# Performance work log

Hardware: AMD Instinct MI355X
Metric: run time of the kernel (lower is better)

## Reference

```python
import jax, jax.numpy as jnp
import numpy as np

B, S, D = 4, 4096, 1024          # batch, seq, d_model
K, H, A = 32, 4, 2               # mem_key_dim, mem_hashes, mem_assoc
T, NB = 65536, 16                # mem_buckets = 2**NB
Dm, Tv = 64, 32                  # mem_dim, mem_vsa_dim
READ_TEMP, VSA_W = 1.0, 1.0
TANH_SCALE, BETA, NOV_THR = 1.0, 1.0, 0.0
WRITE_THR, ETA = 0.5, 0.1


def setup_inputs() -> dict:
    key = jax.random.key(0)
    k = jax.random.split(key, 12)
    s = 0.02
    return {
        "u": jax.random.normal(k[0], (B, S, D), jnp.float32),
        "Wq": jax.random.normal(k[1], (K, D), jnp.float32) * s,
        "Ww": jax.random.normal(k[2], (K, D), jnp.float32) * s,
        "Wv": jax.random.normal(k[3], (Dm, D), jnp.float32) * s,
        "Wout": jax.random.normal(k[4], (D, Dm), jnp.float32) * s,
        "Wg": jax.random.normal(k[5], (1, D), jnp.float32) * s,
        "bg": jnp.zeros((1,), jnp.float32),
        "R": jax.random.normal(k[6], (H, K, NB), jnp.float32),
        "P": jax.random.normal(k[7], (Tv, K), jnp.float32) / np.float32(np.sqrt(K)),
        "mem_keys": jax.random.normal(k[8], (T, A, K), jnp.float32),
        "mem_vals": jax.random.normal(k[9], (T, A, Dm), jnp.float32),
        "mem_tags": jnp.tanh(jax.random.normal(k[10], (T, A, Tv), jnp.float32)),
    }


def reference(u, Wq, Ww, Wv, Wout, Wg, bg, R, P, mem_keys, mem_vals, mem_tags):
    # --- routing (BitRouter): sign bits of random projections -> bucket per hash ---
    q = jnp.einsum('bsd,kd->bsk', u, Wq)                              # query tag
    bits = (jnp.einsum('bsk,hkn->bshn', q, R) > 0).astype(jnp.int32)
    pw = 2 ** jnp.arange(NB, dtype=jnp.int32)
    idx = jnp.sum(bits * pw, axis=-1)                                 # [B,S,H] in [0,T)

    # --- read: gather bucket slots, key + VSA-tag scores, softmax over H*A ---
    Kg, Vg, Tg = mem_keys[idx], mem_vals[idx], mem_tags[idx]          # [B,S,H,A,*]
    score = jnp.einsum('bsk,bshak->bsha', q, Kg) / jnp.sqrt(jnp.float32(K))
    qt = jnp.tanh(TANH_SCALE * jnp.einsum('bsk,tk->bst', q, P))       # VSA tag of query
    score = score + VSA_W * jnp.einsum('bst,bshat->bsha', qt, Tg) / Tv
    attn = jax.nn.softmax((score / READ_TEMP).reshape(B, S, H * A), axis=-1)
    attn = attn.reshape(B, S, H, A)
    read = jnp.einsum('bsha,bshad->bsd', attn, Vg)                    # [B,S,Dm]
    y = jnp.einsum('bsm,dm->bsd', read, Wout)                         # [B,S,D]

    # --- write: gate + VSA novelty, blend best-matching slot, scatter-add ---
    wk = jnp.einsum('bsd,kd->bsk', u, Ww)
    v = jnp.einsum('bsd,md->bsm', u, Wv)
    g = jax.nn.sigmoid(jnp.einsum('bsd,od->bso', u, Wg) + bg)[..., 0]  # [B,S]
    wt = jnp.tanh(TANH_SCALE * jnp.einsum('bsk,tk->bst', wk, P))
    match = jnp.einsum('bst,bshat->bsha', wt, Tg) / Tv
    slot = jnp.argmax(match, axis=-1)                                  # [B,S,H]
    nov = jax.nn.sigmoid(BETA * (NOV_THR - jnp.max(match, axis=-1)))   # novelty gate
    w = ETA * (g * (g > WRITE_THR))[..., None] * nov                   # [B,S,H]
    flat = (idx * A + slot).reshape(-1)                                # [B*S*H]

    def blend(table, gathered, target, dim):
        cur = jnp.take_along_axis(gathered, slot[..., None, None], axis=3)[..., 0, :]
        d = (w[..., None] * (target[:, :, None, :] - cur)).reshape(-1, dim)
        return table.reshape(T * A, dim).at[flat].add(d).reshape(T, A, dim)

    new_keys = blend(mem_keys, Kg, wk, K)
    new_vals = blend(mem_vals, Vg, v, Dm)
    new_tags = blend(mem_tags, Tg, wt, Tv)
    return y, new_keys, new_vals, new_tags
```

## Files before the change

### kernel.cpp

```cpp
#include <hip/hip_runtime.h>
#include <hip/hip_bf16.h>
#include <cstdint>

#define BB 4
#define SS 4096
#define DD 1024
#define KK 32
#define HH 4
#define AA 2
#define TT 65536
#define NBB 16
#define DM 64
#define TV 32
#define MTOK (BB*SS)

__global__ __launch_bounds__(512) void proj_kernel(
    const float* __restrict__ u, const float* __restrict__ Wq,
    const float* __restrict__ Ww, const float* __restrict__ Wv,
    const float* __restrict__ Wg,
    float* __restrict__ q_o, float* __restrict__ wk_o,
    float* __restrict__ v_o, float* __restrict__ g_o)
{
    __shared__ float u_t[64][68];
    __shared__ float w_t[129][68];
    const int t  = threadIdx.x;
    const int m0 = blockIdx.x * 64;
    const int ty = t >> 5;
    const int tx = t & 31;

    float acc[4][5];
#pragma unroll
    for (int i = 0; i < 4; i++)
#pragma unroll
        for (int j = 0; j < 5; j++) acc[i][j] = 0.f;

    for (int k0 = 0; k0 < DD; k0 += 64) {
        __syncthreads();
#pragma unroll
        for (int i = 0; i < 2; i++) {
            int e = t + i * 512;
            int r = e >> 4, cv = e & 15;
            float4 val = *(const float4*)(u + (size_t)(m0 + r) * DD + k0 + cv * 4);
            *(float4*)&u_t[r][cv * 4] = val;
        }
#pragma unroll
        for (int i = 0; i < 5; i++) {
            int e = t + i * 512;
            if (e < 2064) {
                int c = e >> 4, cv = e & 15;
                const float* wrow = (c < 32)  ? (Wq + (size_t)c * DD)
                                  : (c < 64)  ? (Ww + (size_t)(c - 32) * DD)
                                  : (c < 128) ? (Wv + (size_t)(c - 64) * DD)
                                              : Wg;
                float4 val = *(const float4*)(wrow + k0 + cv * 4);
                *(float4*)&w_t[c][cv * 4] = val;
            }
        }
        __syncthreads();
#pragma unroll
        for (int k4 = 0; k4 < 16; k4++) {
            float4 a4[4], b4[5];
#pragma unroll
            for (int i = 0; i < 4; i++) a4[i] = *(const float4*)&u_t[ty * 4 + i][k4 * 4];
#pragma unroll
            for (int j = 0; j < 4; j++) b4[j] = *(const float4*)&w_t[tx + j * 32][k4 * 4];
            b4[4] = *(const float4*)&w_t[128][k4 * 4];
#pragma unroll
            for (int i = 0; i < 4; i++)
#pragma unroll
                for (int j = 0; j < 5; j++) {
                    acc[i][j] = fmaf(a4[i].x, b4[j].x, acc[i][j]);
                    acc[i][j] = fmaf(a4[i].y, b4[j].y, acc[i][j]);
                    acc[i][j] = fmaf(a4[i].z, b4[j].z, acc[i][j]);
                    acc[i][j] = fmaf(a4[i].w, b4[j].w, acc[i][j]);
                }
        }
    }
#pragma unroll
    for (int i = 0; i < 4; i++) {
        int m = m0 + ty * 4 + i;
#pragma unroll
        for (int j = 0; j < 5; j++) {
            int c = tx + j * 32;
            if (c < 32)        q_o[(size_t)m * KK + c]        = acc[i][j];
            else if (c < 64)   wk_o[(size_t)m * KK + (c - 32)] = acc[i][j];
            else if (c < 128)  v_o[(size_t)m * DM + (c - 64)]  = acc[i][j];
            else if (tx == 0)  g_o[m] = acc[i][4];
        }
    }
}

__global__ __launch_bounds__(256) void route_kernel(
    const float* __restrict__ R, const float* __restrict__ P,
    const float* __restrict__ mem_keys, const float* __restrict__ mem_vals,
    const float* __restrict__ mem_tags, const float* __restrict__ bg,
    const float* __restrict__ q_i, const float* __restrict__ wk_i,
    const float* __restrict__ g_i,
    float* __restrict__ read_o, float* __restrict__ wt_o,
    int* __restrict__ idx_o, int* __restrict__ slot_o, float* __restrict__ w_o)
{
    __shared__ float R_s[HH * KK * NBB];
    __shared__ float P_s[TV][KK + 1];
    __shared__ float q_s[4][KK], wk_s[4][KK], qt_s[4][TV], wt_s[4][TV];
    __shared__ float kg_s[4][8][KK], tg_s[4][8][TV], vg_s[4][8][DM];
    __shared__ float sc_s[4][8], mt_s[4][8];
    __shared__ int   idx_s[4][HH];

    const int t    = threadIdx.x;
    const int wid  = t >> 6;
    const int lane = t & 63;
    const int tok  = blockIdx.x * 4 + wid;

    for (int e = t; e < HH * KK * NBB; e += 256) R_s[e] = R[e];
    for (int e = t; e < TV * KK; e += 256) P_s[e >> 5][e & 31] = P[e];

    if (lane < 32) q_s[wid][lane] = q_i[(size_t)tok * KK + lane];
    else           wk_s[wid][lane - 32] = wk_i[(size_t)tok * KK + (lane - 32)];
    __syncthreads();

    {
        int h = lane >> 4, n = lane & 15;
        float s = 0.f;
#pragma unroll
        for (int k = 0; k < KK; k++) s = fmaf(q_s[wid][k], R_s[h * (KK * NBB) + k * NBB + n], s);
        unsigned long long m = __ballot(s > 0.f);
        if (n == 0) {
            int idx = (int)((m >> (h * 16)) & 0xFFFFull);
            idx_s[wid][h] = idx;
            idx_o[(size_t)tok * HH + h] = idx;
        }
    }
    if (lane < 32) {
        float s = 0.f;
#pragma unroll
        for (int k = 0; k < KK; k++) s = fmaf(q_s[wid][k], P_s[lane][k], s);
        qt_s[wid][lane] = tanhf(s);
    } else {
        int t2 = lane - 32;
        float s = 0.f;
#pragma unroll
        for (int k = 0; k < KK; k++) s = fmaf(wk_s[wid][k], P_s[t2][k], s);
        float wtv = tanhf(s);
        wt_s[wid][t2] = wtv;
        wt_o[(size_t)tok * TV + t2] = wtv;
    }
    __syncthreads();

    {
        int p = lane >> 3, j = lane & 7;
        int h = p >> 1, a = p & 1;
        size_t sb = (size_t)idx_s[wid][h] * AA + a;
        *(float4*)&kg_s[wid][p][j * 4] = *(const float4*)(mem_keys + sb * KK + j * 4);
        *(float4*)&tg_s[wid][p][j * 4] = *(const float4*)(mem_tags + sb * TV + j * 4);
        *(float4*)&vg_s[wid][p][j * 8]     = *(const float4*)(mem_vals + sb * DM + j * 8);
        *(float4*)&vg_s[wid][p][j * 8 + 4] = *(const float4*)(mem_vals + sb * DM + j * 8 + 4);
    }
    __syncthreads();

    if (lane < 8) {
        int p = lane;
        float s1 = 0.f, s2 = 0.f;
#pragma unroll
        for (int k = 0; k < KK; k++) s1 = fmaf(q_s[wid][k], kg_s[wid][p][k], s1);
#pragma unroll
        for (int k = 0; k < TV; k++) s2 = fmaf(qt_s[wid][k], tg_s[wid][p][k], s2);
        sc_s[wid][p] = s1 * 0.17677669529663688f + s2 * (1.0f / 32.0f);
    } else if (lane < 16) {
        int p = lane - 8;
        float s2 = 0.f;
#pragma unroll
        for (int k = 0; k < TV; k++) s2 = fmaf(wt_s[wid][k], tg_s[wid][p][k], s2);
        mt_s[wid][p] = s2 * (1.0f / 32.0f);
    }
    __syncthreads();

    {
        float sc[8];
#pragma unroll
        for (int p = 0; p < 8; p++) sc[p] = sc_s[wid][p];
        float mx = sc[0];
#pragma unroll
        for (int p = 1; p < 8; p++) mx = fmaxf(mx, sc[p]);
        float e[8], den = 0.f;
#pragma unroll
        for (int p = 0; p < 8; p++) { e[p] = expf(sc[p] - mx); den += e[p]; }
        float inv = 1.f / den;
        float r = 0.f;
#pragma unroll
        for (int p = 0; p < 8; p++) r = fmaf(e[p] * inv, vg_s[wid][p][lane], r);
        read_o[(size_t)tok * DM + lane] = r;
    }
    if (lane < HH) {
        int h = lane;
        float m0v = mt_s[wid][h * 2], m1v = mt_s[wid][h * 2 + 1];
        int sl = (m1v > m0v) ? 1 : 0;
        float mm = fmaxf(m0v, m1v);
        float nov = 1.f / (1.f + expf(mm));
        float gd = g_i[tok] + bg[0];
        float gg = 1.f / (1.f + expf(-gd));
        float wv = (gg > 0.5f) ? (0.1f * gg * nov) : 0.f;
        slot_o[(size_t)tok * HH + h] = sl;
        w_o[(size_t)tok * HH + h] = wv;
    }
}

__global__ __launch_bounds__(256) void ygemm_kernel(
    const float* __restrict__ read_i, const float* __restrict__ Wout,
    float* __restrict__ y_o)
{
    __shared__ float rd_t[64][68];
    __shared__ float wo_t[64][68];
    const int t  = threadIdx.x;
    const int m0 = blockIdx.x * 64;
    const int n0 = blockIdx.y * 64;
#pragma unroll
    for (int i = 0; i < 4; i++) {
        int e = t + i * 256;
        int r = e >> 4, cv = e & 15;
        *(float4*)&rd_t[r][cv * 4] = *(const float4*)(read_i + (size_t)(m0 + r) * DM + cv * 4);
        *(float4*)&wo_t[r][cv * 4] = *(const float4*)(Wout  + (size_t)(n0 + r) * DM + cv * 4);
    }
    __syncthreads();
    const int ty = t >> 4;
    const int tx = t & 15;
    float acc[4][4];
#pragma unroll
    for (int i = 0; i < 4; i++)
#pragma unroll
        for (int j = 0; j < 4; j++) acc[i][j] = 0.f;
#pragma unroll
    for (int k4 = 0; k4 < 16; k4++) {
        float4 a4[4], b4[4];
#pragma unroll
        for (int i = 0; i < 4; i++) a4[i] = *(const float4*)&rd_t[ty * 4 + i][k4 * 4];
#pragma unroll
        for (int j = 0; j < 4; j++) b4[j] = *(const float4*)&wo_t[tx + j * 16][k4 * 4];
#pragma unroll
        for (int i = 0; i < 4; i++)
#pragma unroll
            for (int j = 0; j < 4; j++) {
                acc[i][j] = fmaf(a4[i].x, b4[j].x, acc[i][j]);
                acc[i][j] = fmaf(a4[i].y, b4[j].y, acc[i][j]);
                acc[i][j] = fmaf(a4[i].z, b4[j].z, acc[i][j]);
                acc[i][j] = fmaf(a4[i].w, b4[j].w, acc[i][j]);
            }
    }
#pragma unroll
    for (int i = 0; i < 4; i++) {
        size_t row = (size_t)(m0 + ty * 4 + i) * DD + n0;
#pragma unroll
        for (int j = 0; j < 4; j++) y_o[row + tx + j * 16] = acc[i][j];
    }
}

__global__ __launch_bounds__(256) void scatter_kernel(
    const float* __restrict__ mem_keys, const float* __restrict__ mem_vals,
    const float* __restrict__ mem_tags,
    const float* __restrict__ wk_i, const float* __restrict__ v_i,
    const float* __restrict__ wt_i,
    const int* __restrict__ idx_i, const int* __restrict__ slot_i,
    const float* __restrict__ w_i,
    float* __restrict__ keys_o, float* __restrict__ vals_o, float* __restrict__ tags_o)
{
    int op   = blockIdx.x * 8 + (threadIdx.x >> 5);
    int lane = threadIdx.x & 31;
    float w = w_i[op];
    if (w == 0.f) return;
    int tok = op >> 2;
    size_t flat = (size_t)idx_i[op] * AA + slot_i[op];
    {
        float d = w * (wk_i[(size_t)tok * KK + lane] - mem_keys[flat * KK + lane]);
        atomicAdd(keys_o + flat * KK + lane, d);
    }
    {
        float d = w * (wt_i[(size_t)tok * TV + lane] - mem_tags[flat * TV + lane]);
        atomicAdd(tags_o + flat * TV + lane, d);
    }
#pragma unroll
    for (int h2 = 0; h2 < 2; h2++) {
        int d2 = lane + h2 * 32;
        float d = w * (v_i[(size_t)tok * DM + d2] - mem_vals[flat * DM + d2]);
        atomicAdd(vals_o + flat * DM + d2, d);
    }
}

extern "C" void kernel_launch(void* const* d_in, const int* in_sizes, int n_in,
                              void* d_out, int out_size, void* d_ws, size_t ws_size,
                              hipStream_t stream)
{
    (void)in_sizes; (void)n_in; (void)out_size; (void)ws_size;
    const float* u    = (const float*)d_in[0];
    const float* Wq   = (const float*)d_in[1];
    const float* Ww   = (const float*)d_in[2];
    const float* Wv   = (const float*)d_in[3];
    const float* Wout = (const float*)d_in[4];
    const float* Wg   = (const float*)d_in[5];
    const float* bg   = (const float*)d_in[6];
    const float* R    = (const float*)d_in[7];
    const float* P    = (const float*)d_in[8];
    const float* mem_keys = (const float*)d_in[9];
    const float* mem_vals = (const float*)d_in[10];
    const float* mem_tags = (const float*)d_in[11];

    float* ws    = (float*)d_ws;
    float* q_w   = ws;
    float* wk_w  = q_w  + (size_t)MTOK * KK;
    float* v_w   = wk_w + (size_t)MTOK * KK;
    float* g_w   = v_w  + (size_t)MTOK * DM;
    float* read_w= g_w  + MTOK;
    float* wt_w  = read_w + (size_t)MTOK * DM;
    float* w_w   = wt_w + (size_t)MTOK * TV;
    int*   idx_w = (int*)(w_w + (size_t)MTOK * HH);
    int*   slot_w= idx_w + (size_t)MTOK * HH;

    float* y_o    = (float*)d_out;
    float* keys_o = y_o    + (size_t)MTOK * DD;
    float* vals_o = keys_o + (size_t)TT * AA * KK;
    float* tags_o = vals_o + (size_t)TT * AA * DM;

    hipMemcpyAsync(keys_o, mem_keys, (size_t)TT * AA * KK * sizeof(float), hipMemcpyDeviceToDevice, stream);
    hipMemcpyAsync(vals_o, mem_vals, (size_t)TT * AA * DM * sizeof(float), hipMemcpyDeviceToDevice, stream);
    hipMemcpyAsync(tags_o, mem_tags, (size_t)TT * AA * TV * sizeof(float), hipMemcpyDeviceToDevice, stream);

    proj_kernel<<<MTOK / 64, 512, 0, stream>>>(u, Wq, Ww, Wv, Wg, q_w, wk_w, v_w, g_w);
    route_kernel<<<MTOK / 4, 256, 0, stream>>>(R, P, mem_keys, mem_vals, mem_tags, bg,
                                               q_w, wk_w, g_w, read_w, wt_w, idx_w, slot_w, w_w);
    ygemm_kernel<<<dim3(MTOK / 64, DD / 64), 256, 0, stream>>>(read_w, Wout, y_o);
    scatter_kernel<<<MTOK * HH / 8, 256, 0, stream>>>(mem_keys, mem_vals, mem_tags,
        wk_w, v_w, wt_w, idx_w, slot_w, w_w, keys_o, vals_o, tags_o);
}
```

Measured before the change: 427.3 us.

## Split-K projection GEMM with larger tiles, partials staged in output buffer

The projection kernel now uses 128x128 tiles with 8x8 register blocking and splits the D reduction four ways across blocks. Partial sums are written into the y output region, which serves as scratch, and the route and scatter kernels sum the partials when they read them. The gate dot product moves into the u-load loop, and the route kernel handles four tokens per wave with wave-local LDS fences instead of block barriers. The y GEMM now runs after scatter so the partial buffers stay valid until they are consumed. The aim is to fill the GPU better with a small-N GEMM and cut barrier overhead, at the cost of extra partial-sum traffic and redundant reductions.

Result: faster. 370.9 us (-13.2%).

```diff
diff --git a/kernel.cpp b/kernel.cpp
--- a/kernel.cpp
+++ b/kernel.cpp
@@ -13,62 +13,67 @@
 #define DM 64
 #define TV 32
 #define MTOK (BB*SS)
-
-__global__ __launch_bounds__(512) void proj_kernel(
+#define PKS 4
+#define PKL (DD/PKS)
+
+#define WAVE_FENCE() asm volatile("s_waitcnt lgkmcnt(0)" ::: "memory")
+
+__global__ __launch_bounds__(256, 2) void proj_kernel(
     const float* __restrict__ u, const float* __restrict__ Wq,
     const float* __restrict__ Ww, const float* __restrict__ Wv,
     const float* __restrict__ Wg,
-    float* __restrict__ q_o, float* __restrict__ wk_o,
-    float* __restrict__ v_o, float* __restrict__ g_o)
-{
-    __shared__ float u_t[64][68];
-    __shared__ float w_t[129][68];
+    float* __restrict__ qs, float* __restrict__ wks,
+    float* __restrict__ vs, float* __restrict__ gs)
+{
+    __shared__ float u_t[128][36];
+    __shared__ float w_t[128][36];
     const int t  = threadIdx.x;
-    const int m0 = blockIdx.x * 64;
-    const int ty = t >> 5;
-    const int tx = t & 31;
-
-    float acc[4][5];
-#pragma unroll
-    for (int i = 0; i < 4; i++)
-#pragma unroll
-        for (int j = 0; j < 5; j++) acc[i][j] = 0.f;
-
-    for (int k0 = 0; k0 < DD; k0 += 64) {
+    const int mb = blockIdx.x & 127;
+    const int ks = blockIdx.x >> 7;
+    const int m0 = mb * 128;
+    const int kb = ks * PKL;
+    const int r0 = t >> 3;
+    const int c8 = t & 7;
+    const int ty = t >> 4;
+    const int tx = t & 15;
+
+    float acc[8][8];
+#pragma unroll
+    for (int i = 0; i < 8; i++)
+#pragma unroll
+        for (int j = 0; j < 8; j++) acc[i][j] = 0.f;
+    float gp[4] = {0.f, 0.f, 0.f, 0.f};
+
+    for (int k0 = 0; k0 < PKL; k0 += 32) {
+        const float4 wg4 = *(const float4*)(Wg + kb + k0 + c8 * 4);
         __syncthreads();
 #pragma unroll
-        for (int i = 0; i < 2; i++) {
-            int e = t + i * 512;
-            int r = e >> 4, cv = e & 15;
-            float4 val = *(const float4*)(u + (size_t)(m0 + r) * DD + k0 + cv * 4);
-            *(float4*)&u_t[r][cv * 4] = val;
-        }
-#pragma unroll
-        for (int i = 0; i < 5; i++) {
-            int e = t + i * 512;
-            if (e < 2064) {
-                int c = e >> 4, cv = e & 15;
-                const float* wrow = (c < 32)  ? (Wq + (size_t)c * DD)
-                                  : (c < 64)  ? (Ww + (size_t)(c - 32) * DD)
-                                  : (c < 128) ? (Wv + (size_t)(c - 64) * DD)
-                                              : Wg;
-                float4 val = *(const float4*)(wrow + k0 + cv * 4);
-                *(float4*)&w_t[c][cv * 4] = val;
-            }
+        for (int p = 0; p < 4; p++) {
+            int r = r0 + 32 * p;
+            float4 uv = *(const float4*)(u + (size_t)(m0 + r) * DD + kb + k0 + c8 * 4);
+            *(float4*)&u_t[r][c8 * 4] = uv;
+            gp[p] = fmaf(uv.x, wg4.x, fmaf(uv.y, wg4.y, fmaf(uv.z, wg4.z, fmaf(uv.w, wg4.w, gp[p]))));
+        }
+#pragma unroll
+        for (int p = 0; p < 4; p++) {
+            int c = r0 + 32 * p;
+            const float* wrow = (c < 32)  ? (Wq + (size_t)c * DD)
+                              : (c < 64)  ? (Ww + (size_t)(c - 32) * DD)
+                                          : (Wv + (size_t)(c - 64) * DD);
+            *(float4*)&w_t[c][c8 * 4] = *(const float4*)(wrow + kb + k0 + c8 * 4);
         }
         __syncthreads();
 #pragma unroll
-        for (int k4 = 0; k4 < 16; k4++) {
-            float4 a4[4], b4[5];
-#pragma unroll
-            for (int i = 0; i < 4; i++) a4[i] = *(const float4*)&u_t[ty * 4 + i][k4 * 4];
-#pragma unroll
-            for (int j = 0; j < 4; j++) b4[j] = *(const float4*)&w_t[tx + j * 32][k4 * 4];
-            b4[4] = *(const float4*)&w_t[128][k4 * 4];
-#pragma unroll
-            for (int i = 0; i < 4; i++)
-#pragma unroll
-                for (int j = 0; j < 5; j++) {
+        for (int k4 = 0; k4 < 8; k4++) {
+            float4 a4[8], b4[8];
+#pragma unroll
+            for (int i = 0; i < 8; i++) a4[i] = *(const float4*)&u_t[ty + 16 * i][k4 * 4];
+#pragma unroll
+            for (int j = 0; j < 8; j++) b4[j] = *(const float4*)&w_t[tx + 16 * j][k4 * 4];
+#pragma unroll
+            for (int i = 0; i < 8; i++)
+#pragma unroll
+                for (int j = 0; j < 8; j++) {
                     acc[i][j] = fmaf(a4[i].x, b4[j].x, acc[i][j]);
                     acc[i][j] = fmaf(a4[i].y, b4[j].y, acc[i][j]);
                     acc[i][j] = fmaf(a4[i].z, b4[j].z, acc[i][j]);
@@ -77,15 +82,23 @@
         }
     }
 #pragma unroll
-    for (int i = 0; i < 4; i++) {
-        int m = m0 + ty * 4 + i;
-#pragma unroll
-        for (int j = 0; j < 5; j++) {
-            int c = tx + j * 32;
-            if (c < 32)        q_o[(size_t)m * KK + c]        = acc[i][j];
-            else if (c < 64)   wk_o[(size_t)m * KK + (c - 32)] = acc[i][j];
-            else if (c < 128)  v_o[(size_t)m * DM + (c - 64)]  = acc[i][j];
-            else if (tx == 0)  g_o[m] = acc[i][4];
+    for (int p = 0; p < 4; p++) {
+        gp[p] += __shfl_xor(gp[p], 1);
+        gp[p] += __shfl_xor(gp[p], 2);
+        gp[p] += __shfl_xor(gp[p], 4);
+    }
+    if (c8 == 0) {
+#pragma unroll
+        for (int p = 0; p < 4; p++) gs[(size_t)ks * MTOK + m0 + r0 + 32 * p] = gp[p];
+    }
+#pragma unroll
+    for (int i = 0; i < 8; i++) {
+        int row = m0 + ty + 16 * i;
+#pragma unroll
+        for (int j = 0; j < 8; j++) {
+            if (j < 2)      qs[(size_t)ks * MTOK * KK + (size_t)row * KK + tx + 16 * j]        = acc[i][j];
+            else if (j < 4) wks[(size_t)ks * MTOK * KK + (size_t)row * KK + tx + 16 * (j - 2)] = acc[i][j];
+            else            vs[(size_t)ks * MTOK * DM + (size_t)row * DM + tx + 16 * (j - 4)]  = acc[i][j];
         }
     }
 }
@@ -94,12 +107,12 @@
     const float* __restrict__ R, const float* __restrict__ P,
     const float* __restrict__ mem_keys, const float* __restrict__ mem_vals,
     const float* __restrict__ mem_tags, const float* __restrict__ bg,
-    const float* __restrict__ q_i, const float* __restrict__ wk_i,
-    const float* __restrict__ g_i,
+    const float* __restrict__ qs, const float* __restrict__ wks,
+    const float* __restrict__ gsl,
     float* __restrict__ read_o, float* __restrict__ wt_o,
     int* __restrict__ idx_o, int* __restrict__ slot_o, float* __restrict__ w_o)
 {
-    __shared__ float R_s[HH * KK * NBB];
+    __shared__ float R_s[4 * 528];
     __shared__ float P_s[TV][KK + 1];
     __shared__ float q_s[4][KK], wk_s[4][KK], qt_s[4][TV], wt_s[4][TV];
     __shared__ float kg_s[4][8][KK], tg_s[4][8][TV], vg_s[4][8][DM];
@@ -109,98 +122,111 @@
     const int t    = threadIdx.x;
     const int wid  = t >> 6;
     const int lane = t & 63;
-    const int tok  = blockIdx.x * 4 + wid;
-
-    for (int e = t; e < HH * KK * NBB; e += 256) R_s[e] = R[e];
+
+    for (int e = t; e < 2048; e += 256) R_s[(e >> 9) * 528 + (e & 511)] = R[e];
     for (int e = t; e < TV * KK; e += 256) P_s[e >> 5][e & 31] = P[e];
-
-    if (lane < 32) q_s[wid][lane] = q_i[(size_t)tok * KK + lane];
-    else           wk_s[wid][lane - 32] = wk_i[(size_t)tok * KK + (lane - 32)];
+    const float bgv = bg[0];
     __syncthreads();
 
-    {
-        int h = lane >> 4, n = lane & 15;
-        float s = 0.f;
-#pragma unroll
-        for (int k = 0; k < KK; k++) s = fmaf(q_s[wid][k], R_s[h * (KK * NBB) + k * NBB + n], s);
-        unsigned long long m = __ballot(s > 0.f);
-        if (n == 0) {
-            int idx = (int)((m >> (h * 16)) & 0xFFFFull);
-            idx_s[wid][h] = idx;
-            idx_o[(size_t)tok * HH + h] = idx;
-        }
-    }
-    if (lane < 32) {
-        float s = 0.f;
-#pragma unroll
-        for (int k = 0; k < KK; k++) s = fmaf(q_s[wid][k], P_s[lane][k], s);
-        qt_s[wid][lane] = tanhf(s);
-    } else {
-        int t2 = lane - 32;
-        float s = 0.f;
-#pragma unroll
-        for (int k = 0; k < KK; k++) s = fmaf(wk_s[wid][k], P_s[t2][k], s);
-        float wtv = tanhf(s);
-        wt_s[wid][t2] = wtv;
-        wt_o[(size_t)tok * TV + t2] = wtv;
-    }
-    __syncthreads();
-
-    {
-        int p = lane >> 3, j = lane & 7;
-        int h = p >> 1, a = p & 1;
-        size_t sb = (size_t)idx_s[wid][h] * AA + a;
-        *(float4*)&kg_s[wid][p][j * 4] = *(const float4*)(mem_keys + sb * KK + j * 4);
-        *(float4*)&tg_s[wid][p][j * 4] = *(const float4*)(mem_tags + sb * TV + j * 4);
-        *(float4*)&vg_s[wid][p][j * 8]     = *(const float4*)(mem_vals + sb * DM + j * 8);
-        *(float4*)&vg_s[wid][p][j * 8 + 4] = *(const float4*)(mem_vals + sb * DM + j * 8 + 4);
-    }
-    __syncthreads();
-
-    if (lane < 8) {
-        int p = lane;
-        float s1 = 0.f, s2 = 0.f;
-#pragma unroll
-        for (int k = 0; k < KK; k++) s1 = fmaf(q_s[wid][k], kg_s[wid][p][k], s1);
-#pragma unroll
-        for (int k = 0; k < TV; k++) s2 = fmaf(qt_s[wid][k], tg_s[wid][p][k], s2);
-        sc_s[wid][p] = s1 * 0.17677669529663688f + s2 * (1.0f / 32.0f);
-    } else if (lane < 16) {
-        int p = lane - 8;
-        float s2 = 0.f;
-#pragma unroll
-        for (int k = 0; k < TV; k++) s2 = fmaf(wt_s[wid][k], tg_s[wid][p][k], s2);
-        mt_s[wid][p] = s2 * (1.0f / 32.0f);
-    }
-    __syncthreads();
-
-    {
-        float sc[8];
-#pragma unroll
-        for (int p = 0; p < 8; p++) sc[p] = sc_s[wid][p];
-        float mx = sc[0];
-#pragma unroll
-        for (int p = 1; p < 8; p++) mx = fmaxf(mx, sc[p]);
-        float e[8], den = 0.f;
-#pragma unroll
-        for (int p = 0; p < 8; p++) { e[p] = expf(sc[p] - mx); den += e[p]; }
-        float inv = 1.f / den;
-        float r = 0.f;
-#pragma unroll
-        for (int p = 0; p < 8; p++) r = fmaf(e[p] * inv, vg_s[wid][p][lane], r);
-        read_o[(size_t)tok * DM + lane] = r;
-    }
-    if (lane < HH) {
-        int h = lane;
-        float m0v = mt_s[wid][h * 2], m1v = mt_s[wid][h * 2 + 1];
-        int sl = (m1v > m0v) ? 1 : 0;
-        float mm = fmaxf(m0v, m1v);
-        float nov = 1.f / (1.f + expf(mm));
-        float gd = g_i[tok] + bg[0];
-        float gg = 1.f / (1.f + expf(-gd));
-        float wv = (gg > 0.5f) ? (0.1f * gg * nov) : 0.f;
-        slot_o[(size_t)tok * HH + h] = sl;
-        w_o[(size_t)tok * HH + h] = wv;
+    for (int ti = 0; ti < 4; ti++) {
+        const int tok = blockIdx.x * 16 + wid * 4 + ti;
+        if (lane < 32) {
+            float s = 0.f;
+#pragma unroll
+            for (int sl = 0; sl < PKS; sl++) s += qs[(size_t)sl * MTOK * KK + (size_t)tok * KK + lane];
+            q_s[wid][lane] = s;
+        } else {
+            int l2 = lane - 32;
+            float s = 0.f;
+#pragma unroll
+            for (int sl = 0; sl < PKS; sl++) s += wks[(size_t)sl * MTOK * KK + (size_t)tok * KK + l2];
+            wk_s[wid][l2] = s;
+        }
+        WAVE_FENCE();
+        {
+            int h = lane >> 4, n = lane & 15;
+            float s = 0.f;
+#pragma unroll
+            for (int k = 0; k < KK; k++) s = fmaf(q_s[wid][k], R_s[h * 528 + k * 16 + n], s);
+            unsigned long long m = __ballot(s > 0.f);
+            if (n == 0) {
+                int idx = (int)((m >> (h * 16)) & 0xFFFFull);
+                idx_s[wid][h] = idx;
+                idx_o[(size_t)tok * HH + h] = idx;
+            }
+        }
+        if (lane < 32) {
+            float s = 0.f;
+#pragma unroll
+            for (int k = 0; k < KK; k++) s = fmaf(q_s[wid][k], P_s[lane][k], s);
+            qt_s[wid][lane] = tanhf(s);
+        } else {
+            int t2 = lane - 32;
+            float s = 0.f;
+#pragma unroll
+            for (int k = 0; k < KK; k++) s = fmaf(wk_s[wid][k], P_s[t2][k], s);
+            float wtv = tanhf(s);
+            wt_s[wid][t2] = wtv;
+            wt_o[(size_t)tok * TV + t2] = wtv;
+        }
+        WAVE_FENCE();
+        {
+            int p = lane >> 3, j = lane & 7;
+            int h = p >> 1, a = p & 1;
+            size_t sb = (size_t)idx_s[wid][h] * AA + a;
+            *(float4*)&kg_s[wid][p][j * 4] = *(const float4*)(mem_keys + sb * KK + j * 4);
+            *(float4*)&tg_s[wid][p][j * 4] = *(const float4*)(mem_tags + sb * TV + j * 4);
+            *(float4*)&vg_s[wid][p][j * 8]     = *(const float4*)(mem_vals + sb * DM + j * 8);
+            *(float4*)&vg_s[wid][p][j * 8 + 4] = *(const float4*)(mem_vals + sb * DM + j * 8 + 4);
+        }
+        WAVE_FENCE();
+        if (lane < 8) {
+            int p = lane;
+            float s1 = 0.f, s2 = 0.f;
+#pragma unroll
+            for (int k = 0; k < KK; k++) s1 = fmaf(q_s[wid][k], kg_s[wid][p][k], s1);
+#pragma unroll
+            for (int k = 0; k < TV; k++) s2 = fmaf(qt_s[wid][k], tg_s[wid][p][k], s2);
+            sc_s[wid][p] = s1 * 0.17677669529663688f + s2 * (1.0f / 32.0f);
+        } else if (lane < 16) {
+            int p = lane - 8;
+            float s2 = 0.f;
+#pragma unroll
+            for (int k = 0; k < TV; k++) s2 = fmaf(wt_s[wid][k], tg_s[wid][p][k], s2);
+            mt_s[wid][p] = s2 * (1.0f / 32.0f);
+        }
+        WAVE_FENCE();
+        {
+            float sc[8];
+#pragma unroll
+            for (int p = 0; p < 8; p++) sc[p] = sc_s[wid][p];
+            float mx = sc[0];
+#pragma unroll
+            for (int p = 1; p < 8; p++) mx = fmaxf(mx, sc[p]);
+            float e[8], den = 0.f;
+#pragma unroll
+            for (int p = 0; p < 8; p++) { e[p] = expf(sc[p] - mx); den += e[p]; }
+            float inv = 1.f / den;
+            float r = 0.f;
+#pragma unroll
+            for (int p = 0; p < 8; p++) r = fmaf(e[p] * inv, vg_s[wid][p][lane], r);
+            read_o[(size_t)tok * DM + lane] = r;
+        }
+        if (lane < HH) {
+            int h = lane;
+            float m0v = mt_s[wid][h * 2], m1v = mt_s[wid][h * 2 + 1];
+            int sl = (m1v > m0v) ? 1 : 0;
+            float mm = fmaxf(m0v, m1v);
+            float nov = 1.f / (1.f + expf(mm));
+            float gd = bgv;
+#pragma unroll
+            for (int s2 = 0; s2 < PKS; s2++) gd += gsl[(size_t)s2 * MTOK + tok];
+            float gg = 1.f / (1.f + expf(-gd));
+            float wv = (gg > 0.5f) ? (0.1f * gg * nov) : 0.f;
+            slot_o[(size_t)tok * HH + h] = sl;
+            w_o[(size_t)tok * HH + h] = wv;
+        }
+        WAVE_FENCE();
     }
 }
 
@@ -256,7 +282,7 @@
 __global__ __launch_bounds__(256) void scatter_kernel(
     const float* __restrict__ mem_keys, const float* __restrict__ mem_vals,
     const float* __restrict__ mem_tags,
-    const float* __restrict__ wk_i, const float* __restrict__ v_i,
+    const float* __restrict__ wks, const float* __restrict__ vsl,
     const float* __restrict__ wt_i,
     const int* __restrict__ idx_i, const int* __restrict__ slot_i,
     const float* __restrict__ w_i,
@@ -269,7 +295,10 @@
     int tok = op >> 2;
     size_t flat = (size_t)idx_i[op] * AA + slot_i[op];
     {
-        float d = w * (wk_i[(size_t)tok * KK + lane] - mem_keys[flat * KK + lane]);
+        float wkv = 0.f;
+#pragma unroll
+        for (int sl = 0; sl < PKS; sl++) wkv += wks[(size_t)sl * MTOK * KK + (size_t)tok * KK + lane];
+        float d = w * (wkv - mem_keys[flat * KK + lane]);
         atomicAdd(keys_o + flat * KK + lane, d);
     }
     {
@@ -279,7 +308,10 @@
 #pragma unroll
     for (int h2 = 0; h2 < 2; h2++) {
         int d2 = lane + h2 * 32;
-        float d = w * (v_i[(size_t)tok * DM + d2] - mem_vals[flat * DM + d2]);
+        float vv = 0.f;
+#pragma unroll
+        for (int sl = 0; sl < PKS; sl++) vv += vsl[(size_t)sl * MTOK * DM + (size_t)tok * DM + d2];
+        float d = w * (vv - mem_vals[flat * DM + d2]);
         atomicAdd(vals_o + flat * DM + d2, d);
     }
 }
@@ -302,30 +334,31 @@
     const float* mem_vals = (const float*)d_in[10];
     const float* mem_tags = (const float*)d_in[11];
 
-    float* ws    = (float*)d_ws;
-    float* q_w   = ws;
-    float* wk_w  = q_w  + (size_t)MTOK * KK;
-    float* v_w   = wk_w + (size_t)MTOK * KK;
-    float* g_w   = v_w  + (size_t)MTOK * DM;
-    float* read_w= g_w  + MTOK;
-    float* wt_w  = read_w + (size_t)MTOK * DM;
-    float* w_w   = wt_w + (size_t)MTOK * TV;
-    int*   idx_w = (int*)(w_w + (size_t)MTOK * HH);
-    int*   slot_w= idx_w + (size_t)MTOK * HH;
-
     float* y_o    = (float*)d_out;
     float* keys_o = y_o    + (size_t)MTOK * DD;
     float* vals_o = keys_o + (size_t)TT * AA * KK;
     float* tags_o = vals_o + (size_t)TT * AA * DM;
 
+    float* qs  = y_o;
+    float* wks = qs  + (size_t)PKS * MTOK * KK;
+    float* vsl = wks + (size_t)PKS * MTOK * KK;
+    float* gsl = vsl + (size_t)PKS * MTOK * DM;
+
+    float* ws     = (float*)d_ws;
+    float* read_w = ws;
+    float* wt_w   = read_w + (size_t)MTOK * DM;
+    float* w_w    = wt_w   + (size_t)MTOK * TV;
+    int*   idx_w  = (int*)(w_w + (size_t)MTOK * HH);
+    int*   slot_w = idx_w + (size_t)MTOK * HH;
+
     hipMemcpyAsync(keys_o, mem_keys, (size_t)TT * AA * KK * sizeof(float), hipMemcpyDeviceToDevice, stream);
     hipMemcpyAsync(vals_o, mem_vals, (size_t)TT * AA * DM * sizeof(float), hipMemcpyDeviceToDevice, stream);
     hipMemcpyAsync(tags_o, mem_tags, (size_t)TT * AA * TV * sizeof(float), hipMemcpyDeviceToDevice, stream);
 
-    proj_kernel<<<MTOK / 64, 512, 0, stream>>>(u, Wq, Ww, Wv, Wg, q_w, wk_w, v_w, g_w);
-    route_kernel<<<MTOK / 4, 256, 0, stream>>>(R, P, mem_keys, mem_vals, mem_tags, bg,
-                                               q_w, wk_w, g_w, read_w, wt_w, idx_w, slot_w, w_w);
+    proj_kernel<<<128 * PKS, 256, 0, stream>>>(u, Wq, Ww, Wv, Wg, qs, wks, vsl, gsl);
+    route_kernel<<<MTOK / 16, 256, 0, stream>>>(R, P, mem_keys, mem_vals, mem_tags, bg,
+                                                qs, wks, gsl, read_w, wt_w, idx_w, slot_w, w_w);
+    scatter_kernel<<<MTOK * HH / 8, 256, 0, stream>>>(mem_keys, mem_vals, mem_tags,
+        wks, vsl, wt_w, idx_w, slot_w, w_w, keys_o, vals_o, tags_o);
     ygemm_kernel<<<dim3(MTOK / 64, DD / 64), 256, 0, stream>>>(read_w, Wout, y_o);
-    scatter_kernel<<<MTOK * HH / 8, 256, 0, stream>>>(mem_keys, mem_vals, mem_tags,
-        wk_w, v_w, wt_w, idx_w, slot_w, w_w, keys_o, vals_o, tags_o);
-}
+}
```
